# Optimization experiments

Measured on AMD Instinct MI355X. Metric: run time of the kernel, lower is better.

The kernel has to match this reference:

```python
import jax, jax.numpy as jnp
import numpy as np

INPUT_DIM = 1024
HIDDEN_DIM = 2048
LATENT_DIM = 256
NUM_EMBEDDINGS = 8192
COMMITMENT_COST = 0.25
BATCH = 16384


def setup_inputs() -> dict:
    key = jax.random.key(0)
    ks = jax.random.split(key, 10)
    def lin(k, fan_in, fan_out):
        # torch nn.Linear default init: U(-1/sqrt(fan_in), 1/sqrt(fan_in))
        bound = 1.0 / np.sqrt(fan_in)
        kw, kb = jax.random.split(k)
        W = jax.random.uniform(kw, (fan_in, fan_out), jnp.float32, -bound, bound)
        b = jax.random.uniform(kb, (fan_out,), jnp.float32, -bound, bound)
        return W, b
    enc_w1, enc_b1 = lin(ks[0], INPUT_DIM, HIDDEN_DIM)
    enc_w2, enc_b2 = lin(ks[1], HIDDEN_DIM, LATENT_DIM)
    dec_w1, dec_b1 = lin(ks[2], LATENT_DIM, HIDDEN_DIM)
    dec_w2, dec_b2 = lin(ks[3], HIDDEN_DIM, INPUT_DIM)
    # codebook init: U(-1/K, 1/K)
    codebook = jax.random.uniform(ks[4], (NUM_EMBEDDINGS, LATENT_DIM), jnp.float32,
                                  -1.0 / NUM_EMBEDDINGS, 1.0 / NUM_EMBEDDINGS)
    x = jax.random.uniform(ks[5], (BATCH, INPUT_DIM), jnp.float32)
    return {"x": x,
            "enc_w1": enc_w1, "enc_b1": enc_b1, "enc_w2": enc_w2, "enc_b2": enc_b2,
            "codebook": codebook,
            "dec_w1": dec_w1, "dec_b1": dec_b1, "dec_w2": dec_w2, "dec_b2": dec_b2}


def reference(x, enc_w1, enc_b1, enc_w2, enc_b2, codebook,
              dec_w1, dec_b1, dec_w2, dec_b2):
    # Encoder: relu(x W1 + b1) W2 + b2 -> z [N, latent]
    h = jax.nn.relu(x @ enc_w1 + enc_b1)
    z = h @ enc_w2 + enc_b2

    # Vector quantizer: squared-L2 distances to codebook [N, K]
    d = (jnp.sum(z * z, axis=1, keepdims=True)
         + jnp.sum(codebook * codebook, axis=1)
         - 2.0 * (z @ codebook.T))
    idx = jnp.argmin(d, axis=1)          # [N] int
    z_q = codebook[idx]                   # gather [N, latent]

    vq_loss = jnp.mean((jax.lax.stop_gradient(z_q) - z) ** 2)
    commit_loss = COMMITMENT_COST * jnp.mean((z_q - jax.lax.stop_gradient(z)) ** 2)
    loss = vq_loss + commit_loss

    # straight-through estimator
    z_q = z + jax.lax.stop_gradient(z_q - z)

    # Decoder: sigmoid(relu(z_q Wd1 + bd1) Wd2 + bd2)
    hd = jax.nn.relu(z_q @ dec_w1 + dec_b1)
    x_recon = jax.nn.sigmoid(hd @ dec_w2 + dec_b2)
    return (x_recon, loss)
```

## Files before the change

kernel.cpp:

```cpp
#include <hip/hip_runtime.h>
#include <math.h>

typedef unsigned short u16;
typedef __bf16 bf16x8 __attribute__((ext_vector_type(8)));
typedef float  f32x4  __attribute__((ext_vector_type(4)));

constexpr int B_  = 16384;
constexpr int DIN = 1024;
constexpr int DH  = 2048;
constexpr int DL  = 256;
constexpr int NE  = 8192;

__device__ __forceinline__ u16 f2bf(float f) {
    union { float f; unsigned u; } v; v.f = f;
    unsigned r = v.u + 0x7fffu + ((v.u >> 16) & 1u);
    return (u16)(r >> 16);
}
__device__ __forceinline__ float bf2f(u16 h) {
    union { unsigned u; float f; } v; v.u = ((unsigned)h) << 16;
    return v.f;
}

#define GLD16(gp, lp)                                                  \
    __builtin_amdgcn_global_load_lds(                                  \
        (__attribute__((address_space(1))) void*)(gp),                 \
        (__attribute__((address_space(3))) void*)(lp), 16, 0, 0)

#define SCHED0() __builtin_amdgcn_sched_barrier(0)
#define BARRIER() do { SCHED0(); __builtin_amdgcn_s_barrier(); SCHED0(); } while (0)
#define WAITV0() asm volatile("s_waitcnt vmcnt(0)" ::: "memory")
#define WAITV3() asm volatile("s_waitcnt vmcnt(3)" ::: "memory")

__device__ __forceinline__ void dev_cast(const float* __restrict__ in,
                                         u16* __restrict__ out, long blk)
{
    const size_t i = ((size_t)blk * 256 + threadIdx.x) * 4;
    float4 v = *(const float4*)(in + i);
    ushort4 o;
    o.x = f2bf(v.x); o.y = f2bf(v.y); o.z = f2bf(v.z); o.w = f2bf(v.w);
    *(ushort4*)(out + i) = o;
}

__device__ __forceinline__ void dev_transpose(const float* __restrict__ in,
                                              u16* __restrict__ out,
                                              int R, int C, long bx, long by,
                                              float (*t)[33])
{
    const int tx = threadIdx.x & 31, ty = threadIdx.x >> 5;
#pragma unroll
    for (int p = 0; p < 4; ++p)
        t[ty + p * 8][tx] = in[(by * 32 + ty + p * 8) * (long)C + bx * 32 + tx];
    __syncthreads();
#pragma unroll
    for (int p = 0; p < 4; ++p)
        out[(bx * 32 + ty + p * 8) * (long)R + by * 32 + tx] = f2bf(t[tx][ty + p * 8]);
}

__global__ __launch_bounds__(256)
void prep_fused(const float* __restrict__ x,   u16* __restrict__ x_bf,
                const float* __restrict__ cb,  u16* __restrict__ cb_bf,
                const float* __restrict__ ew1, u16* __restrict__ w1t,
                const float* __restrict__ ew2, u16* __restrict__ w2t,
                const float* __restrict__ dw1, u16* __restrict__ wd1t,
                const float* __restrict__ dw2, u16* __restrict__ wd2t,
                float* __restrict__ cn2)
{
    __shared__ float t[32][33];
    const long b = blockIdx.x;

    if (b < 16384) {
        dev_cast(x, x_bf, b);
    } else if (b < 18432) {
        dev_cast(cb, cb_bf, b - 16384);
    } else if (b < 20480) {
        const long r = b - 18432;
        dev_transpose(ew1, w1t, DIN, DH, r % 64, r / 64, t);
    } else if (b < 20992) {
        const long r = b - 20480;
        dev_transpose(ew2, w2t, DH, DL, r % 8, r / 8, t);
    } else if (b < 21504) {
        const long r = b - 20992;
        dev_transpose(dw1, wd1t, DL, DH, r % 64, r / 64, t);
    } else if (b < 23552) {
        const long r = b - 21504;
        dev_transpose(dw2, wd2t, DH, DIN, r % 32, r / 32, t);
    } else {
        const long r = b - 23552;
        const int code = (int)((r * 256 + threadIdx.x) >> 6);
        const int lane = threadIdx.x & 63;
        float4 v = *(const float4*)(cb + (long)code * DL + lane * 4);
        float s = fmaf(v.x, v.x, fmaf(v.y, v.y, fmaf(v.z, v.z, v.w * v.w)));
#pragma unroll
        for (int off = 32; off; off >>= 1) s += __shfl_down(s, off);
        if (lane == 0) cn2[code] = 0.5f * s;
    }
}

template <int EPI>
__global__ __launch_bounds__(512, 4)
void gemm_big_bf16(const u16* __restrict__ A, const u16* __restrict__ Bt,
                   const float* __restrict__ bias, void* __restrict__ Cout,
                   int M, int N, int K)
{
    __shared__ __align__(16) u16 As[3 * 8192];
    __shared__ __align__(16) u16 Bs[3 * 4096];

    const int tid = threadIdx.x;
    const int w = tid >> 6, l = tid & 63;
    const int wm = w >> 1, wn = w & 1;

    const int nbx   = N >> 7;
    const int nwg   = (M >> 8) * nbx;
    const int chunk = nwg >> 3;
    const int wg    = ((int)blockIdx.x & 7) * chunk + ((int)blockIdx.x >> 3);
    const long by   = wg / nbx;
    const long bx   = wg % nbx;

    const int lr  = l >> 2;
    const int lsw = (l & 3) ^ ((l >> 3) & 3);
    const int lg  = l >> 4, lm = l & 15;
    const int sx  = (lm >> 1) & 3;

    const u16* Abase = A  + (size_t)(by * 256) * K;
    const u16* Bbase = Bt + (size_t)(bx * 128) * K;

    f32x4 acc[4][4] = {};

    auto stage = [&](int k0, int b) {
        u16* dA = As + b * 8192;
        u16* dB = Bs + b * 4096;
#pragma unroll
        for (int i = 0; i < 2; ++i) {
            const int seg = w * 2 + i;
            GLD16(Abase + (size_t)(seg * 16 + lr) * K + k0 + lsw * 8,
                  dA + seg * 512);
        }
        GLD16(Bbase + (size_t)(w * 16 + lr) * K + k0 + lsw * 8,
              dB + w * 512);
    };

    const int NT = K >> 5;
    stage(0, 0);
    stage(32, 1);

    int cur = 0, pre = 2;
    for (int t = 0; t < NT; ++t) {
        if (t + 1 < NT) { WAITV3(); } else { WAITV0(); }
        BARRIER();
        if (t + 2 < NT) stage((t + 2) << 5, pre);

        const u16* as = As + cur * 8192;
        const u16* bs = Bs + cur * 4096;
        bf16x8 af[4], bfr[4];
#pragma unroll
        for (int m = 0; m < 4; ++m) {
            const int R = wm * 64 + m * 16 + lm;
            af[m] = *(const bf16x8*)&as[R * 32 + ((lg ^ sx) * 8)];
        }
#pragma unroll
        for (int n = 0; n < 4; ++n) {
            const int R = wn * 64 + n * 16 + lm;
            bfr[n] = *(const bf16x8*)&bs[R * 32 + ((lg ^ sx) * 8)];
        }
#pragma unroll
        for (int m = 0; m < 4; ++m)
#pragma unroll
            for (int n = 0; n < 4; ++n)
                acc[m][n] = __builtin_amdgcn_mfma_f32_16x16x32_bf16(
                    af[m], bfr[n], acc[m][n], 0, 0, 0);

        cur = (cur == 2) ? 0 : cur + 1;
        pre = (pre == 2) ? 0 : pre + 1;
    }

#pragma unroll
    for (int n = 0; n < 4; ++n) {
        const long col = bx * 128 + wn * 64 + n * 16 + lm;
        const float bb = bias[col];
#pragma unroll
        for (int m = 0; m < 4; ++m) {
#pragma unroll
            for (int j = 0; j < 4; ++j) {
                const long row = by * 256 + wm * 64 + m * 16 + lg * 4 + j;
                float e = acc[m][n][j] + bb;
                if (EPI == 1) e = fmaxf(e, 0.f);
                ((u16*)Cout)[row * (long)N + col] = f2bf(e);
            }
        }
    }
}

__device__ __forceinline__ void gemm64_core(
    const u16* __restrict__ A, const u16* __restrict__ Bt,
    const float* __restrict__ bias, void* __restrict__ Cout,
    int M, int N, int K, int epi, int bid,
    u16* __restrict__ As, u16* __restrict__ Bs)
{
    const int tid = threadIdx.x;
    const int w = tid >> 6, l = tid & 63;

    const int nbx   = N >> 7;
    const int nwg   = (M >> 6) * nbx;
    const int chunk = nwg >> 3;
    const int wg    = (bid & 7) * chunk + (bid >> 3);
    const long by   = wg / nbx;
    const long bx   = wg % nbx;

    const int lr  = l >> 2;
    const int lsw = (l & 3) ^ ((l >> 3) & 3);
    const int lg  = l >> 4, lm = l & 15;
    const int sx  = (lm >> 1) & 3;

    const u16* Abase = A  + (size_t)(by * 64) * K;
    const u16* Bbase = Bt + (size_t)(bx * 128) * K;

    f32x4 acc[4][2] = {};

    auto stage = [&](int k0, int b) {
        u16* dA = As + b * 2048;
        u16* dB = Bs + b * 4096;
        GLD16(Abase + (size_t)(w * 16 + lr) * K + k0 + lsw * 8, dA + w * 512);
#pragma unroll
        for (int i = 0; i < 2; ++i) {
            const int seg = w * 2 + i;
            GLD16(Bbase + (size_t)(seg * 16 + lr) * K + k0 + lsw * 8,
                  dB + seg * 512);
        }
    };

    const int NT = K >> 5;
    stage(0, 0);
    stage(32, 1);

    int cur = 0, pre = 2;
    for (int t = 0; t < NT; ++t) {
        if (t + 1 < NT) { WAITV3(); } else { WAITV0(); }
        BARRIER();
        if (t + 2 < NT) stage((t + 2) << 5, pre);

        const u16* as = As + cur * 2048;
        const u16* bs = Bs + cur * 4096;
        bf16x8 af[4], bfr[2];
#pragma unroll
        for (int m = 0; m < 4; ++m)
            af[m] = *(const bf16x8*)&as[(m * 16 + lm) * 32 + ((lg ^ sx) * 8)];
#pragma unroll
        for (int n = 0; n < 2; ++n) {
            const int R = w * 32 + n * 16 + lm;
            bfr[n] = *(const bf16x8*)&bs[R * 32 + ((lg ^ sx) * 8)];
        }
#pragma unroll
        for (int m = 0; m < 4; ++m)
#pragma unroll
            for (int n = 0; n < 2; ++n)
                acc[m][n] = __builtin_amdgcn_mfma_f32_16x16x32_bf16(
                    af[m], bfr[n], acc[m][n], 0, 0, 0);

        cur = (cur == 2) ? 0 : cur + 1;
        pre = (pre == 2) ? 0 : pre + 1;
    }

#pragma unroll
    for (int n = 0; n < 2; ++n) {
        const long col = bx * 128 + w * 32 + n * 16 + lm;
        const float bb = bias[col];
#pragma unroll
        for (int m = 0; m < 4; ++m) {
#pragma unroll
            for (int j = 0; j < 4; ++j) {
                const long row = by * 64 + m * 16 + lg * 4 + j;
                float e = acc[m][n][j] + bb;
                if (epi == 1) e = fmaxf(e, 0.f);
                if (epi == 2) {
                    e = 1.f / (1.f + expf(-e));
                    ((float*)Cout)[row * (long)N + col] = e;
                } else {
                    ((u16*)Cout)[row * (long)N + col] = f2bf(e);
                }
            }
        }
    }
}

__global__ __launch_bounds__(256, 4)
void gemm2_dec1_fused(const u16* __restrict__ h,  const u16* __restrict__ w2t,
                      const float* __restrict__ eb2, u16* __restrict__ z,
                      const u16* __restrict__ cb, const u16* __restrict__ wd1t,
                      const float* __restrict__ db1, u16* __restrict__ hcode)
{
    __shared__ __align__(16) u16 As[3 * 2048];
    __shared__ __align__(16) u16 Bs[3 * 4096];
    const int b = (int)blockIdx.x;
    if (b < 512)
        gemm64_core(h, w2t, eb2, z, B_, DL, DH, 0, b, As, Bs);
    else
        gemm64_core(cb, wd1t, db1, hcode, NE, DH, DL, 1, b - 512, As, Bs);
}

__global__ __launch_bounds__(256, 4)
void gemm_dec2(const u16* __restrict__ hcode, const u16* __restrict__ wd2t,
               const float* __restrict__ db2, float* __restrict__ Xcode)
{
    __shared__ __align__(16) u16 As[3 * 2048];
    __shared__ __align__(16) u16 Bs[3 * 4096];
    gemm64_core(hcode, wd2t, db2, Xcode, NE, DIN, DH, 2, (int)blockIdx.x, As, Bs);
}

__global__ __launch_bounds__(256, 2)
void vq_score2(const u16* __restrict__ z, const u16* __restrict__ cbt,
               const float* __restrict__ cn2,
               float* __restrict__ val8, int* __restrict__ idx8)
{
    __shared__ __align__(16) u16 lds[32768];

    const int tid = threadIdx.x;
    const int w = tid >> 6, l = tid & 63;
    const int rq = blockIdx.x >> 3;
    const int q  = blockIdx.x & 7;

    const int st_row8 = tid >> 5;
    const int st_s    = (tid & 31) ^ st_row8;
    const int lg = l >> 4, lm = l & 15;
    const int swz_x = l & 7;

    bf16x8 af[4][8];
    const long zbase_row = (long)rq * 256;
#pragma unroll
    for (int h = 0; h < 2; ++h) {
#pragma unroll
        for (int i = 0; i < 16; ++i) {
            const int row = i * 8 + st_row8;
            const u16* g = z + (zbase_row + h * 128 + row) * DL + st_s * 8;
            GLD16(g, lds + ((size_t)i * 256 + w * 64) * 8);
        }
        __syncthreads();
        if ((w >> 1) == h) {
            const int lrow0 = (w & 1) * 64;
#pragma unroll
            for (int m = 0; m < 4; ++m) {
                const int lrow = lrow0 + m * 16 + lm;
#pragma unroll
                for (int kg = 0; kg < 8; ++kg) {
                    const int s = (kg * 4 + lg) ^ swz_x;
                    af[m][kg] = *(const bf16x8*)&lds[lrow * 256 + s * 8];
                }
            }
        }
        __syncthreads();
    }

    const int code00 = q * (NE / 8);

    float bestv[16];
    int   besti[16];
#pragma unroll
    for (int k = 0; k < 16; ++k) { bestv[k] = 1e30f; besti[k] = 0; }

    auto stage_tile = [&](int t) {
        const int b = t & 1;
#pragma unroll
        for (int i = 0; i < 8; ++i) {
            const int c = i * 8 + st_row8;
            const u16* g = cbt + (size_t)(code00 + t * 64 + c) * DL + st_s * 8;
            GLD16(g, lds + ((size_t)b * 16384 + ((size_t)i * 256 + w * 64) * 8));
        }
    };

    stage_tile(0);
    __syncthreads();

    for (int t = 0; t < 16; ++t) {
        if (t < 15) stage_tile(t + 1);
        const u16* buf = lds + (size_t)(t & 1) * 16384;

#pragma unroll
        for (int n = 0; n < 4; ++n) {
            const int code_g = code00 + t * 64 + n * 16 + lm;
            const float cn2v = cn2[code_g];
            bf16x8 bfr[8];
#pragma unroll
            for (int kg = 0; kg < 8; ++kg) {
                const int lrow = n * 16 + lm;
                const int s = (kg * 4 + lg) ^ swz_x;
                bfr[kg] = *(const bf16x8*)&buf[lrow * 256 + s * 8];
            }
            f32x4 acc[4] = {};
#pragma unroll
            for (int kg = 0; kg < 8; ++kg)
#pragma unroll
                for (int m = 0; m < 4; ++m)
                    acc[m] = __builtin_amdgcn_mfma_f32_16x16x32_bf16(
                        af[m][kg], bfr[kg], acc[m], 0, 0, 0);
#pragma unroll
            for (int m = 0; m < 4; ++m)
#pragma unroll
                for (int j = 0; j < 4; ++j) {
                    const float s = cn2v - acc[m][j];
                    const int k16 = m * 4 + j;
                    if (s < bestv[k16]) { bestv[k16] = s; besti[k16] = code_g; }
                }
        }
        __syncthreads();
    }

#pragma unroll
    for (int off = 1; off < 16; off <<= 1) {
#pragma unroll
        for (int k = 0; k < 16; ++k) {
            const float ov = __shfl_xor(bestv[k], off);
            const int   oi = __shfl_xor(besti[k], off);
            if (ov < bestv[k] || (ov == bestv[k] && oi < besti[k])) {
                bestv[k] = ov; besti[k] = oi;
            }
        }
    }
    if (lm == 0) {
#pragma unroll
        for (int m = 0; m < 4; ++m)
#pragma unroll
            for (int j = 0; j < 4; ++j) {
                const long row = zbase_row + w * 64 + m * 16 + lg * 4 + j;
                val8[(size_t)q * B_ + row] = bestv[m * 4 + j];
                idx8[(size_t)q * B_ + row] = besti[m * 4 + j];
            }
    }
}

__global__ __launch_bounds__(256)
void vq_select2(const float* __restrict__ val8, const int* __restrict__ idx8,
                const u16* __restrict__ z, const float* __restrict__ cb,
                int* __restrict__ idxf, float* __restrict__ partial)
{
    __shared__ int   s_idx[256];
    __shared__ float s_red[4];
    const int tid = threadIdx.x;
    const long row = (long)blockIdx.x * 256 + tid;

    float bv = val8[row];
    int   bi = idx8[row];
#pragma unroll
    for (int qq = 1; qq < 8; ++qq) {
        const float v = val8[(size_t)qq * B_ + row];
        const int   i = idx8[(size_t)qq * B_ + row];
        if (v < bv || (v == bv && i < bi)) { bv = v; bi = i; }
    }
    s_idx[tid] = bi;
    idxf[row]  = bi;
    __syncthreads();

    float ls = 0.f;
    const int sub = tid & 7;
#pragma unroll
    for (int pass = 0; pass < 8; ++pass) {
        const int rl = pass * 32 + (tid >> 3);
        const int gi = s_idx[rl];
        const long rg = (long)blockIdx.x * 256 + rl;
#pragma unroll
        for (int tt = 0; tt < 8; ++tt) {
            const int d = sub * 4 + tt * 32;
            float4 c4 = *(const float4*)(cb + (long)gi * DL + d);
            ushort4 zu = *(const ushort4*)(z + rg * DL + d);
            const float dx = c4.x - bf2f(zu.x), dy = c4.y - bf2f(zu.y);
            const float dz = c4.z - bf2f(zu.z), dw = c4.w - bf2f(zu.w);
            ls += dx * dx + dy * dy + dz * dz + dw * dw;
        }
    }
#pragma unroll
    for (int off = 32; off; off >>= 1) ls += __shfl_down(ls, off);
    if ((tid & 63) == 0) s_red[tid >> 6] = ls;
    __syncthreads();
    if (tid == 0)
        partial[blockIdx.x] = s_red[0] + s_red[1] + s_red[2] + s_red[3];
}

__global__ __launch_bounds__(256)
void loss_finalize(const float* __restrict__ partial, float* __restrict__ out)
{
    __shared__ float s_red[4];
    const int tid = threadIdx.x;
    float s = (tid < 64) ? partial[tid] : 0.f;
#pragma unroll
    for (int off = 32; off; off >>= 1) s += __shfl_down(s, off);
    if ((tid & 63) == 0) s_red[tid >> 6] = s;
    __syncthreads();
    if (tid == 0)
        out[0] = 1.25f * (s_red[0] + s_red[1] + s_red[2] + s_red[3])
                 / (float)((long)B_ * DL);
}

__global__ __launch_bounds__(256)
void gather_rows(const float* __restrict__ Xcode, const int* __restrict__ idxf,
                 float* __restrict__ out)
{
    const int tid  = threadIdx.x;
    const int lane = tid & 63;
    const long row = (long)blockIdx.x * 4 + (tid >> 6);
    const long gi  = idxf[row];
    const float* src = Xcode + gi * DIN;
    float*       dst = out + row * DIN;
#pragma unroll
    for (int t = 0; t < 4; ++t) {
        const int d = lane * 4 + t * 256;
        *(float4*)(dst + d) = *(const float4*)(src + d);
    }
}

extern "C" void kernel_launch(void* const* d_in, const int* in_sizes, int n_in,
                              void* d_out, int out_size, void* d_ws, size_t ws_size,
                              hipStream_t stream)
{
    const float* x   = (const float*)d_in[0];
    const float* ew1 = (const float*)d_in[1];
    const float* eb1 = (const float*)d_in[2];
    const float* ew2 = (const float*)d_in[3];
    const float* eb2 = (const float*)d_in[4];
    const float* cbk = (const float*)d_in[5];
    const float* dw1 = (const float*)d_in[6];
    const float* db1 = (const float*)d_in[7];
    const float* dw2 = (const float*)d_in[8];
    const float* db2 = (const float*)d_in[9];
    float* out = (float*)d_out;

    char* p = (char*)d_ws;
    auto alloc = [&](size_t bytes) {
        char* r = p; p += (bytes + 255) & ~(size_t)255; return r;
    };
    u16*   x_bf  = (u16*)alloc((size_t)B_ * DIN * 2);
    u16*   h_bf  = (u16*)alloc((size_t)B_ * DH * 2);
    u16*   z_bf  = (u16*)alloc((size_t)B_ * DL * 2);
    u16*   cb_bf = (u16*)alloc((size_t)NE * DL * 2);
    u16*   w1t   = (u16*)alloc((size_t)DH * DIN * 2);
    u16*   w2t   = (u16*)alloc((size_t)DL * DH * 2);
    u16*   wd1t  = (u16*)alloc((size_t)DH * DL * 2);
    u16*   wd2t  = (u16*)alloc((size_t)DIN * DH * 2);
    float* Xcode = (float*)alloc((size_t)NE * DIN * 4);
    float* cn2   = (float*)alloc((size_t)NE * 4);
    float* val8  = (float*)alloc((size_t)8 * B_ * 4);
    int*   idx8  = (int*)alloc((size_t)8 * B_ * 4);
    int*   idxf  = (int*)alloc((size_t)B_ * 4);
    float* part  = (float*)alloc(64 * 4);

    u16* hcode = x_bf;

    prep_fused<<<25600, 256, 0, stream>>>(x, x_bf, cbk, cb_bf,
                                          ew1, w1t, ew2, w2t,
                                          dw1, wd1t, dw2, wd2t, cn2);

    gemm_big_bf16<1><<<(B_ / 256) * (DH / 128), 512, 0, stream>>>(
        x_bf, w1t, eb1, h_bf, B_, DH, DIN);

    gemm2_dec1_fused<<<2560, 256, 0, stream>>>(h_bf, w2t, eb2, z_bf,
                                               cb_bf, wd1t, db1, hcode);

    gemm_dec2<<<(NE / 64) * (DIN / 128), 256, 0, stream>>>(
        hcode, wd2t, db2, Xcode);

    vq_score2<<<512, 256, 0, stream>>>(z_bf, cb_bf, cn2, val8, idx8);
    vq_select2<<<B_ / 256, 256, 0, stream>>>(val8, idx8, z_bf, cbk, idxf, part);
    loss_finalize<<<1, 256, 0, stream>>>(part, out + (size_t)B_ * DIN);

    gather_rows<<<B_ / 4, 256, 0, stream>>>(Xcode, idxf, out);
}
```

Measured before the change: 294.0 us.

## Triple-buffer VQ codebook tiles, stage norms in LDS, fuse loss finalize into gather

The VQ scoring kernel now uses 32-code tiles in a three-deep LDS ring with vmcnt-based waits and one barrier per tile, replacing the double buffer with a trailing sync. This lets loads for tile t+2 overlap compute on tile t. Codebook norms are prefetched into LDS once rather than read from global memory per tile. The loss-finalize kernel is merged into the gather kernel as an extra block, which removes one launch. Smaller tiles mean more barriers and loop iterations, and the vmcnt counts must exactly match the number of issued loads for correctness.

```diff
diff --git a/kernel.cpp b/kernel.cpp
--- a/kernel.cpp
+++ b/kernel.cpp
@@ -30,6 +30,7 @@
 #define BARRIER() do { SCHED0(); __builtin_amdgcn_s_barrier(); SCHED0(); } while (0)
 #define WAITV0() asm volatile("s_waitcnt vmcnt(0)" ::: "memory")
 #define WAITV3() asm volatile("s_waitcnt vmcnt(3)" ::: "memory")
+#define WAITV4() asm volatile("s_waitcnt vmcnt(4)" ::: "memory")
 
 __device__ __forceinline__ void dev_cast(const float* __restrict__ in,
                                          u16* __restrict__ out, long blk)
@@ -307,7 +308,7 @@
 }
 
 __global__ __launch_bounds__(256, 2)
-void vq_score2(const u16* __restrict__ z, const u16* __restrict__ cbt,
+void vq_score3(const u16* __restrict__ z, const u16* __restrict__ cbt,
                const float* __restrict__ cn2,
                float* __restrict__ val8, int* __restrict__ idx8)
 {
@@ -350,6 +351,9 @@
     }
 
     const int code00 = q * (NE / 8);
+    const float* cn2s = (const float*)(lds + 24576);
+
+    GLD16(cn2 + code00 + (size_t)w * 256, lds + 24576 + w * 512);
 
     float bestv[16];
     int   besti[16];
@@ -357,26 +361,28 @@
     for (int k = 0; k < 16; ++k) { bestv[k] = 1e30f; besti[k] = 0; }
 
     auto stage_tile = [&](int t) {
-        const int b = t & 1;
-#pragma unroll
-        for (int i = 0; i < 8; ++i) {
+        const int b = t % 3;
+#pragma unroll
+        for (int i = 0; i < 4; ++i) {
             const int c = i * 8 + st_row8;
-            const u16* g = cbt + (size_t)(code00 + t * 64 + c) * DL + st_s * 8;
-            GLD16(g, lds + ((size_t)b * 16384 + ((size_t)i * 256 + w * 64) * 8));
+            const u16* g = cbt + (size_t)(code00 + t * 32 + c) * DL + st_s * 8;
+            GLD16(g, lds + (size_t)b * 8192 + ((size_t)i * 256 + w * 64) * 8);
         }
     };
 
     stage_tile(0);
-    __syncthreads();
-
-    for (int t = 0; t < 16; ++t) {
-        if (t < 15) stage_tile(t + 1);
-        const u16* buf = lds + (size_t)(t & 1) * 16384;
-
-#pragma unroll
-        for (int n = 0; n < 4; ++n) {
-            const int code_g = code00 + t * 64 + n * 16 + lm;
-            const float cn2v = cn2[code_g];
+    stage_tile(1);
+
+    for (int t = 0; t < 32; ++t) {
+        if (t + 1 < 32) { WAITV4(); } else { WAITV0(); }
+        BARRIER();
+        if (t + 2 < 32) stage_tile(t + 2);
+
+        const u16* buf = lds + (size_t)(t % 3) * 8192;
+#pragma unroll
+        for (int n = 0; n < 2; ++n) {
+            const int code_g = code00 + t * 32 + n * 16 + lm;
+            const float cn2v = cn2s[t * 32 + n * 16 + lm];
             bf16x8 bfr[8];
 #pragma unroll
             for (int kg = 0; kg < 8; ++kg) {
@@ -400,7 +406,6 @@
                     if (s < bestv[k16]) { bestv[k16] = s; besti[k16] = code_g; }
                 }
         }
-        __syncthreads();
     }
 
 #pragma unroll
@@ -474,25 +479,23 @@
 }
 
 __global__ __launch_bounds__(256)
-void loss_finalize(const float* __restrict__ partial, float* __restrict__ out)
-{
-    __shared__ float s_red[4];
+void gather_loss(const float* __restrict__ Xcode, const int* __restrict__ idxf,
+                 const float* __restrict__ partial, float* __restrict__ out,
+                 float* __restrict__ loss_out)
+{
     const int tid = threadIdx.x;
-    float s = (tid < 64) ? partial[tid] : 0.f;
-#pragma unroll
-    for (int off = 32; off; off >>= 1) s += __shfl_down(s, off);
-    if ((tid & 63) == 0) s_red[tid >> 6] = s;
-    __syncthreads();
-    if (tid == 0)
-        out[0] = 1.25f * (s_red[0] + s_red[1] + s_red[2] + s_red[3])
-                 / (float)((long)B_ * DL);
-}
-
-__global__ __launch_bounds__(256)
-void gather_rows(const float* __restrict__ Xcode, const int* __restrict__ idxf,
-                 float* __restrict__ out)
-{
-    const int tid  = threadIdx.x;
+    if (blockIdx.x == 4096) {
+        __shared__ float s_red[4];
+        float s = (tid < 64) ? partial[tid] : 0.f;
+#pragma unroll
+        for (int off = 32; off; off >>= 1) s += __shfl_down(s, off);
+        if ((tid & 63) == 0) s_red[tid >> 6] = s;
+        __syncthreads();
+        if (tid == 0)
+            loss_out[0] = 1.25f * (s_red[0] + s_red[1] + s_red[2] + s_red[3])
+                          / (float)((long)B_ * DL);
+        return;
+    }
     const int lane = tid & 63;
     const long row = (long)blockIdx.x * 4 + (tid >> 6);
     const long gi  = idxf[row];
@@ -555,9 +558,9 @@
     gemm_dec2<<<(NE / 64) * (DIN / 128), 256, 0, stream>>>(
         hcode, wd2t, db2, Xcode);
 
-    vq_score2<<<512, 256, 0, stream>>>(z_bf, cb_bf, cn2, val8, idx8);
+    vq_score3<<<512, 256, 0, stream>>>(z_bf, cb_bf, cn2, val8, idx8);
     vq_select2<<<B_ / 256, 256, 0, stream>>>(val8, idx8, z_bf, cbk, idxf, part);
-    loss_finalize<<<1, 256, 0, stream>>>(part, out + (size_t)B_ * DIN);
-
-    gather_rows<<<B_ / 4, 256, 0, stream>>>(Xcode, idxf, out);
-}
+
+    gather_loss<<<4097, 256, 0, stream>>>(Xcode, idxf, part, out,
+                                          out + (size_t)B_ * DIN);
+}
```

After: 296.7 us (median of 2 runs). Within noise of the previous version (+0.9%).
